# Performance work log

Measured on AMD Instinct MI355X. Metric: run time of the kernel, lower is better.

Reference implementation:

```python
import jax, jax.numpy as jnp
import numpy as np

B, N, F, W = 8, 2048, 128, 64


def setup_inputs() -> dict:
    key = jax.random.key(0)
    k1, k2, k3, k4 = jax.random.split(key, 4)
    x = jax.random.normal(k1, (B, N, F), dtype=jnp.float32)
    adj = jnp.ones((B, N, N), dtype=bool)  # accepted by forward but unused
    w_key = jax.random.normal(k2, (F, W), dtype=jnp.float32) * 0.1
    w_value = jax.random.normal(k3, (F, F), dtype=jnp.float32) * 0.1
    w_query = jax.random.normal(k4, (F, W), dtype=jnp.float32) * 0.1
    return {"x": x, "adj": adj, "w_key": w_key, "w_value": w_value, "w_query": w_query}


def reference(x, adj, w_key, w_value, w_query):
    # keys/queries: [B, N, W]; values: [B, N, F]
    keys = x @ w_key
    querys = x @ w_query
    values = x @ w_value
    # per-batch softmax(Q K^T) over last dim -> [B, N, N]
    scores = jax.nn.softmax(jnp.einsum('bnw,bmw->bnm', querys, keys), axis=-1)
    # original broadcast-multiply-sum is exactly scores @ values
    out = jnp.einsum('bnm,bmf->bnf', scores, values)
    return out
```

## Files before the change

kernel.cpp:

```cpp
#include <hip/hip_runtime.h>
#include <hip/hip_bf16.h>
#include <math.h>

constexpr int B = 8;
constexpr int N = 2048;
constexpr int F = 128;
constexpr int W = 64;

constexpr int TQ = 128;
constexpr int TK = 64;
constexpr int KSPLIT = 4;
constexpr int TILES_PER_SPLIT = (N / TK) / KSPLIT;

typedef short     bf16x8 __attribute__((ext_vector_type(8)));
typedef _Float16  f16x8  __attribute__((ext_vector_type(8)));
typedef float     f32x4  __attribute__((ext_vector_type(4)));
typedef float     f32x16 __attribute__((ext_vector_type(16)));
typedef ushort    u16x8  __attribute__((ext_vector_type(8)));

__device__ inline ushort f2bf(float f) {
  union { float f; uint u; } v; v.f = f;
  uint u = v.u;
  return (ushort)((u + 0x7FFFu + ((u >> 16) & 1u)) >> 16);
}
__device__ inline float bf2f(ushort h) {
  union { uint u; float f; } v; v.u = ((uint)h) << 16;
  return v.f;
}

__device__ inline void lgkm_barrier() {
  asm volatile("s_waitcnt lgkmcnt(0)" ::: "memory");
  __builtin_amdgcn_s_barrier();
}

__global__ __launch_bounds__(256) void prep_w(
    const float* __restrict__ wq, const float* __restrict__ wk,
    const float* __restrict__ wv, _Float16* __restrict__ wt) {
  int gid = blockIdx.x * 256 + threadIdx.x;
  int n = gid >> 4;
  int k0 = (gid & 15) * 8;
  _Float16 t[8];
#pragma unroll
  for (int j = 0; j < 8; ++j) {
    int k = k0 + j;
    float val = (n < 64)  ? wq[k * W + n]
              : (n < 128) ? wk[k * W + (n - 64)]
                          : wv[k * F + (n - 128)];
    t[j] = (_Float16)val;
  }
  *(uint4*)&wt[n * 128 + k0] = *(uint4*)t;
}

constexpr int KP = 136;

__global__ __launch_bounds__(256) void proj_kernel(
    const float* __restrict__ x, const _Float16* __restrict__ wt,
    _Float16* __restrict__ q16, _Float16* __restrict__ k16,
    ushort* __restrict__ vt_ws) {
  __shared__ _Float16 xs[32][KP];

  const int tid  = threadIdx.x;
  const int wid  = tid >> 6;
  const int lane = tid & 63;
  const int lg = lane >> 4, li = lane & 15;
  const int pass = wid >> 1;
  const int rg   = wid & 1;
  const int bx   = blockIdx.x;
  const int b    = bx & 7;
  const int nloc = (bx >> 3) * 32;
  const int brow0 = b * N + nloc;

  for (int idx = tid; idx < 32 * 128 / 4; idx += 256) {
    int row = idx >> 5, c4 = idx & 31;
    float4 xv = *(const float4*)&x[(size_t)(brow0 + row) * F + c4 * 4];
    _Float16 h[4] = {(_Float16)xv.x, (_Float16)xv.y,
                     (_Float16)xv.z, (_Float16)xv.w};
    *(float2*)&xs[row][c4 * 4] = *(float2*)h;
  }
  __syncthreads();

  f16x8 xa[4];
#pragma unroll
  for (int kk = 0; kk < 4; ++kk)
    xa[kk] = *(const f16x8*)&xs[rg * 16 + li][kk * 32 + lg * 8];

  f32x4 zero = {0.f, 0.f, 0.f, 0.f};
  f32x4 acc[8];
#pragma unroll
  for (int t = 0; t < 8; ++t) acc[t] = zero;

  const _Float16* wb = wt + (size_t)pass * 128 * 128;

  if (pass == 0) {
#pragma unroll
    for (int kk = 0; kk < 4; ++kk)
#pragma unroll
      for (int nt = 0; nt < 8; ++nt) {
        f16x8 bw = *(const f16x8*)&wb[(nt * 16 + li) * 128 + kk * 32 + lg * 8];
        acc[nt] = __builtin_amdgcn_mfma_f32_16x16x32_f16(xa[kk], bw, acc[nt], 0, 0, 0);
      }
#pragma unroll
    for (int nt = 0; nt < 8; ++nt)
#pragma unroll
      for (int r = 0; r < 4; ++r) {
        int row = brow0 + rg * 16 + lg * 4 + r;
        int c = nt * 16 + li;
        _Float16 hv = (_Float16)acc[nt][r];
        if (nt < 4) q16[row * W + c] = hv;
        else        k16[row * W + (c - 64)] = hv;
      }
  } else {
#pragma unroll
    for (int kk = 0; kk < 4; ++kk)
#pragma unroll
      for (int mt = 0; mt < 8; ++mt) {
        f16x8 aw = *(const f16x8*)&wb[(mt * 16 + li) * 128 + kk * 32 + lg * 8];
        acc[mt] = __builtin_amdgcn_mfma_f32_16x16x32_f16(aw, xa[kk], acc[mt], 0, 0, 0);
      }
    const int n   = nloc + rg * 16 + li;
    const int kt  = n >> 6;
    const int kk2 = (n >> 4) & 3;
    const int fl  = ((n >> 2) & 1) * 32;
    const int ei  = (n & 3) + 4 * ((n >> 3) & 1);
    ushort* vb = vt_ws + (((size_t)(b * 32 + kt) * 4 + kk2) * 4) * 512;
#pragma unroll
    for (int mt = 0; mt < 8; ++mt)
#pragma unroll
      for (int r = 0; r < 4; ++r) {
        int f = mt * 16 + lg * 4 + r;
        vb[(size_t)(f >> 5) * 512 + (size_t)(fl + (f & 31)) * 8 + ei] =
            f2bf(acc[mt][r]);
      }
  }
}

constexpr int LK = 72;

__global__ __launch_bounds__(256, 2) void attn_kernel(
    const _Float16* __restrict__ q16, const _Float16* __restrict__ k16,
    const ushort* __restrict__ vfr,
    ushort* __restrict__ op0, ushort* __restrict__ op1,
    ushort* __restrict__ op2, ushort* __restrict__ op3,
    float* __restrict__ lsums) {
  __shared__ _Float16 ksh[2][TK][LK];

  const int tid  = threadIdx.x;
  const int wid  = tid >> 6;
  const int lane = tid & 63;
  const int q32  = lane & 31;
  const int hi   = lane >> 5;

  const int hw    = blockIdx.x;
  const int grp   = (hw & 7) | ((hw >> 7) << 3);
  const int qt    = (hw >> 3) & 15;
  const int b     = grp & 7;
  const int split = grp >> 3;

  const size_t koffb = (size_t)b * N * W;
  const ushort* vfb_base = vfr + (size_t)b * 32 * 16 * 512;

  const size_t qrow = (size_t)(b * N + qt * TQ + wid * 32 + q32) * W + hi * 8;
  f16x8 qa[4];
#pragma unroll
  for (int kk = 0; kk < 4; ++kk)
    qa[kk] = *(const f16x8*)&q16[qrow + kk * 16];

  const int krow0 = tid >> 3, krow1 = krow0 + 32, kc8 = tid & 7;
  uint4 kr0, kr1;
  auto load_k = [&](int kt) {
    kr0 = *(const uint4*)&k16[koffb + ((size_t)kt * TK + krow0) * W + kc8 * 8];
    kr1 = *(const uint4*)&k16[koffb + ((size_t)kt * TK + krow1) * W + kc8 * 8];
  };

  float l_lane = 0.f;
  f32x16 oa[4];
#pragma unroll
  for (int ft = 0; ft < 4; ++ft)
#pragma unroll
    for (int r = 0; r < 16; ++r) oa[ft][r] = 0.f;

  const int kt0 = split * TILES_PER_SPLIT;
  load_k(kt0);

  for (int t = 0; t < TILES_PER_SPLIT; ++t) {
    const int kt = kt0 + t;
    const int pb = t & 1;

    const ushort* vfb = vfb_base + (size_t)kt * 16 * 512 + (size_t)lane * 8;
    uint4 vreg[16];
#pragma unroll
    for (int kk2 = 0; kk2 < 4; ++kk2) {
      const ushort* vb2 = vfb + kk2 * 2048;
      vreg[kk2 * 4 + 0] = *(const uint4*)&vb2[0];
      vreg[kk2 * 4 + 1] = *(const uint4*)&vb2[512];
      vreg[kk2 * 4 + 2] = *(const uint4*)&vb2[1024];
      vreg[kk2 * 4 + 3] = *(const uint4*)&vb2[1536];
    }

    *(uint4*)&ksh[pb][krow0][kc8 * 8] = kr0;
    *(uint4*)&ksh[pb][krow1][kc8 * 8] = kr1;
    if (t + 1 < TILES_PER_SPLIT) load_k(kt + 1);

    lgkm_barrier();

    f32x16 s2[2];
#pragma unroll
    for (int mt = 0; mt < 2; ++mt)
#pragma unroll
      for (int r = 0; r < 16; ++r) s2[mt][r] = 0.f;
    __builtin_amdgcn_s_setprio(1);
#pragma unroll
    for (int kk = 0; kk < 4; ++kk)
#pragma unroll
      for (int mt = 0; mt < 2; ++mt) {
        f16x8 kf = *(const f16x8*)&ksh[pb][mt * 32 + q32][kk * 16 + hi * 8];
        s2[mt] = __builtin_amdgcn_mfma_f32_32x32x16_f16(kf, qa[kk], s2[mt], 0, 0, 0);
      }
    __builtin_amdgcn_s_setprio(0);

    uint4 paw[4];
#pragma unroll
    for (int mt = 0; mt < 2; ++mt) {
      float pf[16];
#pragma unroll
      for (int r = 0; r < 16; ++r) pf[r] = __expf(s2[mt][r]);
      float t0 = (pf[0] + pf[1]) + (pf[2] + pf[3]);
      float t1 = (pf[4] + pf[5]) + (pf[6] + pf[7]);
      float t2 = (pf[8] + pf[9]) + (pf[10] + pf[11]);
      float t3 = (pf[12] + pf[13]) + (pf[14] + pf[15]);
      l_lane += (t0 + t1) + (t2 + t3);
#pragma unroll
      for (int gm = 0; gm < 2; ++gm) {
        uint w0, w1, w2, w3;
        asm("v_cvt_pk_bf16_f32 %0, %1, %2" : "=v"(w0) : "v"(pf[gm * 8 + 0]), "v"(pf[gm * 8 + 1]));
        asm("v_cvt_pk_bf16_f32 %0, %1, %2" : "=v"(w1) : "v"(pf[gm * 8 + 2]), "v"(pf[gm * 8 + 3]));
        asm("v_cvt_pk_bf16_f32 %0, %1, %2" : "=v"(w2) : "v"(pf[gm * 8 + 4]), "v"(pf[gm * 8 + 5]));
        asm("v_cvt_pk_bf16_f32 %0, %1, %2" : "=v"(w3) : "v"(pf[gm * 8 + 6]), "v"(pf[gm * 8 + 7]));
        paw[mt * 2 + gm] = make_uint4(w0, w1, w2, w3);
      }
    }

    __builtin_amdgcn_s_setprio(1);
#pragma unroll
    for (int g = 0; g < 4; ++g) {
      bf16x8 pa = __builtin_bit_cast(bf16x8, paw[g]);
#pragma unroll
      for (int ft = 0; ft < 4; ++ft) {
        bf16x8 vf = __builtin_bit_cast(bf16x8, vreg[g * 4 + ft]);
        oa[ft] = __builtin_amdgcn_mfma_f32_32x32x16_bf16(pa, vf, oa[ft], 0, 0, 0);
      }
    }
    __builtin_amdgcn_s_setprio(0);
  }

  l_lane += __shfl_xor(l_lane, 32, 64);

  ushort* opb = (split == 0) ? op0 : (split == 1) ? op1 : (split == 2) ? op2 : op3;
  ushort* ob = opb + (size_t)(b * N + qt * TQ + wid * 32) * F;
#pragma unroll
  for (int ft = 0; ft < 4; ++ft)
#pragma unroll
    for (int r = 0; r < 16; ++r) {
      int qr = (r & 3) + 8 * (r >> 2) + 4 * hi;
      ob[(size_t)qr * F + ft * 32 + q32] = f2bf(oa[ft][r]);
    }
  if (hi == 0) {
    size_t gr = (size_t)split * B * N + (size_t)(b * N + qt * TQ) + wid * 32 + q32;
    lsums[gr] = l_lane;
  }
}

__global__ __launch_bounds__(256) void combine_kernel(
    const ushort* __restrict__ op0, const ushort* __restrict__ op1,
    const ushort* __restrict__ op2, const ushort* __restrict__ op3,
    const float* __restrict__ lsums, float* __restrict__ out) {
  const int bx = blockIdx.x;
  const int gr = (bx & 7) * N + (bx >> 3) * 16 + (threadIdx.x >> 4);
  const int c8 = (threadIdx.x & 15) * 8;
  constexpr size_t BN = (size_t)B * N;
  const float l = lsums[gr] + lsums[BN + gr] + lsums[2 * BN + gr] + lsums[3 * BN + gr];
  const float inv = 1.f / l;
  const size_t base = (size_t)gr * F + c8;
  u16x8 a0 = *(const u16x8*)&op0[base];
  u16x8 a1 = *(const u16x8*)&op1[base];
  u16x8 a2 = *(const u16x8*)&op2[base];
  u16x8 a3 = *(const u16x8*)&op3[base];
  float o[8];
#pragma unroll
  for (int j = 0; j < 8; ++j)
    o[j] = (bf2f(a0[j]) + bf2f(a1[j]) + bf2f(a2[j]) + bf2f(a3[j])) * inv;
  *(float4*)&out[base]     = *(float4*)&o[0];
  *(float4*)&out[base + 4] = *(float4*)&o[4];
}

extern "C" void kernel_launch(void* const* d_in, const int* in_sizes, int n_in,
                              void* d_out, int out_size, void* d_ws, size_t ws_size,
                              hipStream_t stream) {
  const float* x  = (const float*)d_in[0];
  const float* wk = (const float*)d_in[2];
  const float* wv = (const float*)d_in[3];
  const float* wq = (const float*)d_in[4];
  float* out = (float*)d_out;

  constexpr size_t BNW = (size_t)B * N * W;
  constexpr size_t BNF = (size_t)B * N * F;
  _Float16* q16 = (_Float16*)d_ws;
  _Float16* k16 = q16 + BNW;
  ushort*   vt  = (ushort*)(k16 + BNW);
  _Float16* wt  = (_Float16*)(vt + BNF);
  ushort*   op0 = (ushort*)(wt + 32768);
  ushort*   op1 = op0 + BNF;
  ushort*   op2 = op1 + BNF;
  ushort*   op3 = op2 + BNF;
  float*    ls  = (float*)(op3 + BNF);

  prep_w<<<16, 256, 0, stream>>>(wq, wk, wv, wt);
  proj_kernel<<<(B * N) / 32, 256, 0, stream>>>(x, wt, q16, k16, vt);
  attn_kernel<<<dim3(512), 256, 0, stream>>>(q16, k16, vt, op0, op1, op2, op3, ls);
  combine_kernel<<<(B * N) / 16, 256, 0, stream>>>(op0, op1, op2, op3, ls, out);
}
```

Baseline: 207.3 us.

## Fuse split-K combine into attention kernel via in-block LDS reduction

Each 512-thread block now handles 64 query rows, with 8 waves split into 2 query groups and 4 key splits. The partial outputs and row sums are reduced through shared memory and normalized in-kernel, which removes the separate combine kernel and the bf16 partial-output round trip through global memory. K fragments are now loaded directly from global memory into registers instead of being staged in LDS with double buffering. The trade-offs are a grid of only 256 blocks, heavier per-wave global K loads, and extra barriers in the epilogue.

```diff
diff --git a/kernel.cpp b/kernel.cpp
--- a/kernel.cpp
+++ b/kernel.cpp
@@ -7,30 +7,15 @@
 constexpr int F = 128;
 constexpr int W = 64;
 
-constexpr int TQ = 128;
-constexpr int TK = 64;
-constexpr int KSPLIT = 4;
-constexpr int TILES_PER_SPLIT = (N / TK) / KSPLIT;
-
 typedef short     bf16x8 __attribute__((ext_vector_type(8)));
 typedef _Float16  f16x8  __attribute__((ext_vector_type(8)));
 typedef float     f32x4  __attribute__((ext_vector_type(4)));
 typedef float     f32x16 __attribute__((ext_vector_type(16)));
-typedef ushort    u16x8  __attribute__((ext_vector_type(8)));
 
 __device__ inline ushort f2bf(float f) {
   union { float f; uint u; } v; v.f = f;
   uint u = v.u;
   return (ushort)((u + 0x7FFFu + ((u >> 16) & 1u)) >> 16);
-}
-__device__ inline float bf2f(ushort h) {
-  union { uint u; float f; } v; v.u = ((uint)h) << 16;
-  return v.f;
-}
-
-__device__ inline void lgkm_barrier() {
-  asm volatile("s_waitcnt lgkmcnt(0)" ::: "memory");
-  __builtin_amdgcn_s_barrier();
 }
 
 __global__ __launch_bounds__(256) void prep_w(
@@ -134,43 +119,34 @@
   }
 }
 
-constexpr int LK = 72;
-
-__global__ __launch_bounds__(256, 2) void attn_kernel(
+__global__ __launch_bounds__(512, 2) void attn_kernel(
     const _Float16* __restrict__ q16, const _Float16* __restrict__ k16,
-    const ushort* __restrict__ vfr,
-    ushort* __restrict__ op0, ushort* __restrict__ op1,
-    ushort* __restrict__ op2, ushort* __restrict__ op3,
-    float* __restrict__ lsums) {
-  __shared__ _Float16 ksh[2][TK][LK];
+    const ushort* __restrict__ vfr, float* __restrict__ out) {
+  __shared__ float lds_f[4][128][36];
+  __shared__ float ls[4][32];
 
   const int tid  = threadIdx.x;
   const int wid  = tid >> 6;
   const int lane = tid & 63;
   const int q32  = lane & 31;
   const int hi   = lane >> 5;
-
-  const int hw    = blockIdx.x;
-  const int grp   = (hw & 7) | ((hw >> 7) << 3);
-  const int qt    = (hw >> 3) & 15;
-  const int b     = grp & 7;
-  const int split = grp >> 3;
-
-  const size_t koffb = (size_t)b * N * W;
+  const int qg   = wid & 1;
+  const int ks   = wid >> 1;
+
+  const int hw = blockIdx.x;
+  const int b  = hw & 7;
+  const int qt = hw >> 3;
+
   const ushort* vfb_base = vfr + (size_t)b * 32 * 16 * 512;
 
-  const size_t qrow = (size_t)(b * N + qt * TQ + wid * 32 + q32) * W + hi * 8;
+  const size_t qrow = (size_t)(b * N + qt * 64 + qg * 32 + q32) * W + hi * 8;
   f16x8 qa[4];
 #pragma unroll
   for (int kk = 0; kk < 4; ++kk)
     qa[kk] = *(const f16x8*)&q16[qrow + kk * 16];
 
-  const int krow0 = tid >> 3, krow1 = krow0 + 32, kc8 = tid & 7;
-  uint4 kr0, kr1;
-  auto load_k = [&](int kt) {
-    kr0 = *(const uint4*)&k16[koffb + ((size_t)kt * TK + krow0) * W + kc8 * 8];
-    kr1 = *(const uint4*)&k16[koffb + ((size_t)kt * TK + krow1) * W + kc8 * 8];
-  };
+  const _Float16* kb =
+      k16 + (size_t)b * N * W + ((size_t)ks * 512 + q32) * W + hi * 8;
 
   float l_lane = 0.f;
   f32x16 oa[4];
@@ -179,13 +155,15 @@
 #pragma unroll
     for (int r = 0; r < 16; ++r) oa[ft][r] = 0.f;
 
-  const int kt0 = split * TILES_PER_SPLIT;
-  load_k(kt0);
-
-  for (int t = 0; t < TILES_PER_SPLIT; ++t) {
-    const int kt = kt0 + t;
-    const int pb = t & 1;
-
+  for (int t = 0; t < 8; ++t) {
+    f16x8 kf[2][4];
+#pragma unroll
+    for (int mt = 0; mt < 2; ++mt)
+#pragma unroll
+      for (int kk = 0; kk < 4; ++kk)
+        kf[mt][kk] = *(const f16x8*)&kb[(size_t)(t * 64 + mt * 32) * W + kk * 16];
+
+    const int kt = ks * 8 + t;
     const ushort* vfb = vfb_base + (size_t)kt * 16 * 512 + (size_t)lane * 8;
     uint4 vreg[16];
 #pragma unroll
@@ -197,12 +175,6 @@
       vreg[kk2 * 4 + 3] = *(const uint4*)&vb2[1536];
     }
 
-    *(uint4*)&ksh[pb][krow0][kc8 * 8] = kr0;
-    *(uint4*)&ksh[pb][krow1][kc8 * 8] = kr1;
-    if (t + 1 < TILES_PER_SPLIT) load_k(kt + 1);
-
-    lgkm_barrier();
-
     f32x16 s2[2];
 #pragma unroll
     for (int mt = 0; mt < 2; ++mt)
@@ -212,10 +184,8 @@
 #pragma unroll
     for (int kk = 0; kk < 4; ++kk)
 #pragma unroll
-      for (int mt = 0; mt < 2; ++mt) {
-        f16x8 kf = *(const f16x8*)&ksh[pb][mt * 32 + q32][kk * 16 + hi * 8];
-        s2[mt] = __builtin_amdgcn_mfma_f32_32x32x16_f16(kf, qa[kk], s2[mt], 0, 0, 0);
-      }
+      for (int mt = 0; mt < 2; ++mt)
+        s2[mt] = __builtin_amdgcn_mfma_f32_32x32x16_f16(kf[mt][kk], qa[kk], s2[mt], 0, 0, 0);
     __builtin_amdgcn_s_setprio(0);
 
     uint4 paw[4];
@@ -255,42 +225,36 @@
 
   l_lane += __shfl_xor(l_lane, 32, 64);
 
-  ushort* opb = (split == 0) ? op0 : (split == 1) ? op1 : (split == 2) ? op2 : op3;
-  ushort* ob = opb + (size_t)(b * N + qt * TQ + wid * 32) * F;
-#pragma unroll
-  for (int ft = 0; ft < 4; ++ft)
-#pragma unroll
-    for (int r = 0; r < 16; ++r) {
-      int qr = (r & 3) + 8 * (r >> 2) + 4 * hi;
-      ob[(size_t)qr * F + ft * 32 + q32] = f2bf(oa[ft][r]);
-    }
-  if (hi == 0) {
-    size_t gr = (size_t)split * B * N + (size_t)(b * N + qt * TQ) + wid * 32 + q32;
-    lsums[gr] = l_lane;
-  }
-}
-
-__global__ __launch_bounds__(256) void combine_kernel(
-    const ushort* __restrict__ op0, const ushort* __restrict__ op1,
-    const ushort* __restrict__ op2, const ushort* __restrict__ op3,
-    const float* __restrict__ lsums, float* __restrict__ out) {
-  const int bx = blockIdx.x;
-  const int gr = (bx & 7) * N + (bx >> 3) * 16 + (threadIdx.x >> 4);
-  const int c8 = (threadIdx.x & 15) * 8;
-  constexpr size_t BN = (size_t)B * N;
-  const float l = lsums[gr] + lsums[BN + gr] + lsums[2 * BN + gr] + lsums[3 * BN + gr];
-  const float inv = 1.f / l;
-  const size_t base = (size_t)gr * F + c8;
-  u16x8 a0 = *(const u16x8*)&op0[base];
-  u16x8 a1 = *(const u16x8*)&op1[base];
-  u16x8 a2 = *(const u16x8*)&op2[base];
-  u16x8 a3 = *(const u16x8*)&op3[base];
-  float o[8];
-#pragma unroll
-  for (int j = 0; j < 8; ++j)
-    o[j] = (bf2f(a0[j]) + bf2f(a1[j]) + bf2f(a2[j]) + bf2f(a3[j])) * inv;
-  *(float4*)&out[base]     = *(float4*)&o[0];
-  *(float4*)&out[base + 4] = *(float4*)&o[4];
+#pragma unroll
+  for (int rho = 0; rho < 2; ++rho) {
+    if (qg == rho) {
+      if (hi == 0) ls[ks][q32] = l_lane;
+#pragma unroll
+      for (int ft = 0; ft < 4; ++ft)
+#pragma unroll
+        for (int g = 0; g < 4; ++g) {
+          f32x4 v4 = {oa[ft][4 * g + 0], oa[ft][4 * g + 1],
+                      oa[ft][4 * g + 2], oa[ft][4 * g + 3]};
+          *(f32x4*)&lds_f[ks][ft * 32 + q32][8 * g + 4 * hi] = v4;
+        }
+    }
+    __syncthreads();
+    {
+      const int rq = tid & 31;
+      const int f0 = (tid >> 5) * 8;
+      const float ltot = ls[0][rq] + ls[1][rq] + ls[2][rq] + ls[3][rq];
+      const float inv = 1.f / ltot;
+      float o[8];
+#pragma unroll
+      for (int j = 0; j < 8; ++j)
+        o[j] = ((lds_f[0][f0 + j][rq] + lds_f[1][f0 + j][rq]) +
+                (lds_f[2][f0 + j][rq] + lds_f[3][f0 + j][rq])) * inv;
+      float* orow = out + ((size_t)(b * N + qt * 64 + rho * 32 + rq)) * F + f0;
+      *(float4*)&orow[0] = *(float4*)&o[0];
+      *(float4*)&orow[4] = *(float4*)&o[4];
+    }
+    __syncthreads();
+  }
 }
 
 extern "C" void kernel_launch(void* const* d_in, const int* in_sizes, int n_in,
@@ -308,14 +272,8 @@
   _Float16* k16 = q16 + BNW;
   ushort*   vt  = (ushort*)(k16 + BNW);
   _Float16* wt  = (_Float16*)(vt + BNF);
-  ushort*   op0 = (ushort*)(wt + 32768);
-  ushort*   op1 = op0 + BNF;
-  ushort*   op2 = op1 + BNF;
-  ushort*   op3 = op2 + BNF;
-  float*    ls  = (float*)(op3 + BNF);
 
   prep_w<<<16, 256, 0, stream>>>(wq, wk, wv, wt);
   proj_kernel<<<(B * N) / 32, 256, 0, stream>>>(x, wt, q16, k16, vt);
-  attn_kernel<<<dim3(512), 256, 0, stream>>>(q16, k16, vt, op0, op1, op2, op3, ls);
-  combine_kernel<<<(B * N) / 16, 256, 0, stream>>>(op0, op1, op2, op3, ls, out);
-}
+  attn_kernel<<<256, 512, 0, stream>>>(q16, k16, vt, out);
+}
```

After: 214.6 us. 3.5% more time.
